# Kernel tuning notes

Hardware: AMD Instinct MI355X
Metric: run time of the kernel (lower is better)

The kernel has to match this reference:

```python
import jax, jax.numpy as jnp
import numpy as np

FIR = (1.0, 3.0, 3.0, 1.0)

def _fir_kernel():
    k = jnp.array(FIR, dtype=jnp.float32)
    k = jnp.outer(k, k)
    return k / jnp.sum(k)  # gain = 1

def setup_inputs() -> dict:
    key = jax.random.key(0)
    k1, k2, k3 = jax.random.split(key, 3)
    N, C, H, W = 8, 512, 64, 64
    return {
        "hidden_states": jax.random.normal(k1, (N, C, H, W), jnp.float32),
        "weight": jax.random.normal(k2, (512, 512, 3, 3), jnp.float32) * 0.02,
        "bias": jax.random.normal(k3, (512,), jnp.float32) * 0.01,
    }

def reference(hidden_states, weight, bias):
    # FirDownsample2D forward, use_conv=True, factor=2, fir_kernel=(1,3,3,1).
    # pad_value = kH - factor + (convW - 1) = 4 - 2 + 2 = 4 -> pad = (2, 2)
    k = _fir_kernel()  # [4,4], normalized
    C = hidden_states.shape[1]
    # upfirdn2d_native with up=1, down=1: pad spatially then per-channel
    # cross-correlation with the FLIPPED kernel (== true convolution).
    kf = jnp.flip(k, (0, 1)).astype(hidden_states.dtype)
    kf = jnp.broadcast_to(kf[None, None], (C, 1, 4, 4))  # depthwise [C,1,4,4]
    y = jax.lax.conv_general_dilated(
        hidden_states, kf, window_strides=(1, 1), padding=[(2, 2), (2, 2)],
        dimension_numbers=("NCHW", "OIHW", "NCHW"), feature_group_count=C)
    # y: [N, C, H+1, W+1]; fused 3x3 conv, stride=factor=2, no padding.
    out = jax.lax.conv_general_dilated(
        y, weight, window_strides=(2, 2), padding="VALID",
        dimension_numbers=("NCHW", "OIHW", "NCHW"))  # [N, Cout, H//2, W//2]
    return out + bias[None, :, None, None]
```

## Files before the change

### kernel.cpp

```cpp
#include <hip/hip_runtime.h>
#include <stdint.h>

#define CI 512
#define CO 512
#define HI 64
#define WI 64
#define HY 65
#define NB 8

typedef __bf16 bf16x8 __attribute__((ext_vector_type(8)));
typedef float f32x4 __attribute__((ext_vector_type(4)));

__device__ __forceinline__ unsigned short f2bf(float f) {
  unsigned int u = __float_as_uint(f);
  return (unsigned short)((u + 0x7fffu + ((u >> 16) & 1u)) >> 16);
}

__device__ __forceinline__ void async16(void* lds, const void* g) {
  __builtin_amdgcn_global_load_lds(
      (const __attribute__((address_space(1))) uint32_t*)g,
      (__attribute__((address_space(3))) uint32_t*)lds, 16, 0, 0);
}

#define CT 32
#define RT 13

__global__ __launch_bounds__(256) void fir_kernel(const float* __restrict__ x,
                                                  unsigned short* __restrict__ yt) {
  __shared__ float raw[CT][WI + 1];
  __shared__ float hrow[4][HY][CT];

  const int tid = threadIdx.x;
  const int bid = blockIdx.x;
  const int n = bid / 80;
  const int rem = bid % 80;
  const int c0 = (rem / 5) * CT;
  const int r0 = (rem % 5) * RT;

  const float* xb = x + ((size_t)n * CI + c0) * (HI * WI);

  const int lc = tid >> 3;
  const int lq = tid & 7;
  const int c = tid & (CT - 1);
  const int sb = tid >> 5;

  auto stage = [&](int hr) {
    __syncthreads();
    if ((unsigned)hr < (unsigned)HI) {
      const float* rowp = xb + ((size_t)lc * HI + hr) * WI;
      float4 a = *(const float4*)&rowp[lq * 4];
      float4 b = *(const float4*)&rowp[(lq + 8) * 4];
      raw[lc][lq * 4 + 0] = a.x; raw[lc][lq * 4 + 1] = a.y;
      raw[lc][lq * 4 + 2] = a.z; raw[lc][lq * 4 + 3] = a.w;
      raw[lc][(lq + 8) * 4 + 0] = b.x; raw[lc][(lq + 8) * 4 + 1] = b.y;
      raw[lc][(lq + 8) * 4 + 2] = b.z; raw[lc][(lq + 8) * 4 + 3] = b.w;
    }
    __syncthreads();
    const int slot = hr & 3;
    if ((unsigned)hr < (unsigned)HI) {
#pragma unroll
      for (int k = 0; k < 9; k++) {
        const int s = sb + (k << 3);
        if (s < HY) {
          float v = 0.f;
          if (s >= 2) v += raw[c][s - 2];
          if (s >= 1) v += 3.f * raw[c][s - 1];
          if (s <= 63) v += 3.f * raw[c][s];
          if (s <= 62) v += raw[c][s + 1];
          hrow[slot][s][c] = v;
        }
      }
    } else {
#pragma unroll
      for (int k = 0; k < 9; k++) {
        const int s = sb + (k << 3);
        if (s < HY) hrow[slot][s][c] = 0.f;
      }
    }
  };

  stage(r0 - 2);
  stage(r0 - 1);
  stage(r0);

  for (int i = 0; i < RT; i++) {
    const int r = r0 + i;
    stage(r + 1);
    __syncthreads();
    const int q0 = (r - 2) & 3, q1 = (r - 1) & 3, q2 = r & 3, q3 = (r + 1) & 3;
    unsigned short* yo = yt + (((size_t)n * HY + r) * HY) * CI + c0 + c;
#pragma unroll
    for (int k = 0; k < 9; k++) {
      const int s = sb + (k << 3);
      if (s < HY) {
        const float y = (hrow[q0][s][c] + 3.f * hrow[q1][s][c] +
                         3.f * hrow[q2][s][c] + hrow[q3][s][c]) * (1.f / 64.f);
        yo[(size_t)s * CI] = f2bf(y);
      }
    }
  }
}

__global__ __launch_bounds__(256) void wt_kernel(const float* __restrict__ w,
                                                 unsigned short* __restrict__ wtb) {
  const int gid = blockIdx.x * 256 + threadIdx.x;
  const int ci = gid & (CI - 1);
  const int co = gid >> 9;
  const float* src = w + ((size_t)co * CI + ci) * 9;
#pragma unroll
  for (int t = 0; t < 9; t++) {
    wtb[((size_t)t * CO + co) * CI + ci] = f2bf(src[t]);
  }
}

__global__ __launch_bounds__(256) void init_kernel(const float* __restrict__ bias,
                                                   float* __restrict__ out) {
  const int gid = blockIdx.x * 256 + threadIdx.x;
  const float bv = bias[(gid >> 8) & 511];
  float4 v = {bv, bv, bv, bv};
  *(float4*)(out + (size_t)gid * 4) = v;
}

__global__ __launch_bounds__(512, 2) void conv_kernel(
    const unsigned short* __restrict__ wtb,
    const unsigned short* __restrict__ yt,
    float* __restrict__ out) {
  __shared__ unsigned short Alds[3][128 * 64];
  __shared__ unsigned short Blds[3][256 * 64];

  const int tid = threadIdx.x;
  const int xcd = blockIdx.x & 7;
  const int j = blockIdx.x >> 3;
  const int pos_tile = xcd * 4 + (j >> 3);
  const int variant = j & 7;
  const int co_t = (variant >> 1) << 7;
  const int split = variant & 1;
  const int ks0 = split * 36;
  const int m0 = pos_tile << 8;
  const int n = m0 >> 10;

  uint32_t aoff[2];
#pragma unroll
  for (int i = 0; i < 2; i++) {
    const int ch = tid + i * 512;
    const int row = ch >> 3, s = ch & 7;
    aoff[i] = (uint32_t)((co_t + row) * CI + ((s ^ (row & 7)) << 3));
  }
  uint32_t boff[4];
#pragma unroll
  for (int i = 0; i < 4; i++) {
    const int ch = tid + i * 512;
    const int p = ch >> 3, s = ch & 7;
    const int pos = m0 + p;
    const int ho = (pos & 1023) >> 5, wo = pos & 31;
    boff[i] = (uint32_t)(((n * HY + 2 * ho) * HY + 2 * wo) * CI + ((s ^ (p & 7)) << 3));
  }

  auto stg = [&](unsigned short* Ab, unsigned short* Bb, int gks) {
    const int tap = gks >> 3;
    const int ci0 = (gks & 7) << 6;
    const int kh = tap / 3, kw = tap - kh * 3;
    const unsigned short* wsrc = wtb + (size_t)tap * (CO * CI) + ci0;
    const unsigned short* ysrc = yt + (size_t)(kh * HY + kw) * CI + ci0;
#pragma unroll
    for (int i = 0; i < 2; i++)
      async16(Ab + (size_t)(tid + i * 512) * 8, wsrc + aoff[i]);
#pragma unroll
    for (int i = 0; i < 4; i++)
      async16(Bb + (size_t)(tid + i * 512) * 8, ysrc + boff[i]);
  };

  const int wv = tid >> 6;
  const int wcoW = (wv >> 2) << 6;
  const int wposW = (wv & 3) << 6;
  const int l = tid & 63;
  const int ll = l & 15, kg = l >> 4;
  const int a7 = ll & 7;

  int aidx[4][2], bidx[4][2];
#pragma unroll
  for (int m = 0; m < 4; m++)
#pragma unroll
    for (int kk = 0; kk < 2; kk++)
      aidx[m][kk] = (wcoW + m * 16 + ll) * 64 + ((((kk << 2) | kg) ^ a7) << 3);
#pragma unroll
  for (int nf = 0; nf < 4; nf++)
#pragma unroll
    for (int kk = 0; kk < 2; kk++)
      bidx[nf][kk] = (wposW + nf * 16 + ll) * 64 + ((((kk << 2) | kg) ^ a7) << 3);

  f32x4 acc[4][4] = {};

  stg(&Alds[0][0], &Blds[0][0], ks0);
  stg(&Alds[1][0], &Blds[1][0], ks0 + 1);
  asm volatile("s_waitcnt vmcnt(6)" ::: "memory");
  __builtin_amdgcn_s_barrier();

#define COMPUTE(CUR)                                                        \
  {                                                                         \
    const unsigned short* Ac = &Alds[CUR][0];                               \
    const unsigned short* Bc = &Blds[CUR][0];                               \
    _Pragma("unroll") for (int kk = 0; kk < 2; kk++) {                      \
      const bf16x8 a0 = *(const bf16x8*)(Ac + aidx[0][kk]);                 \
      const bf16x8 a1 = *(const bf16x8*)(Ac + aidx[1][kk]);                 \
      const bf16x8 a2 = *(const bf16x8*)(Ac + aidx[2][kk]);                 \
      const bf16x8 a3 = *(const bf16x8*)(Ac + aidx[3][kk]);                 \
      const bf16x8 b0 = *(const bf16x8*)(Bc + bidx[0][kk]);                 \
      const bf16x8 b1 = *(const bf16x8*)(Bc + bidx[1][kk]);                 \
      const bf16x8 b2 = *(const bf16x8*)(Bc + bidx[2][kk]);                 \
      const bf16x8 b3 = *(const bf16x8*)(Bc + bidx[3][kk]);                 \
      __builtin_amdgcn_s_setprio(1);                                        \
      _Pragma("unroll") for (int m = 0; m < 4; m++) {                       \
        const bf16x8 am = (m == 0) ? a0 : (m == 1) ? a1 : (m == 2) ? a2 : a3; \
        acc[m][0] = __builtin_amdgcn_mfma_f32_16x16x32_bf16(am, b0, acc[m][0], 0, 0, 0); \
        acc[m][1] = __builtin_amdgcn_mfma_f32_16x16x32_bf16(am, b1, acc[m][1], 0, 0, 0); \
        acc[m][2] = __builtin_amdgcn_mfma_f32_16x16x32_bf16(am, b2, acc[m][2], 0, 0, 0); \
        acc[m][3] = __builtin_amdgcn_mfma_f32_16x16x32_bf16(am, b3, acc[m][3], 0, 0, 0); \
      }                                                                     \
      __builtin_amdgcn_s_setprio(0);                                        \
    }                                                                       \
  }

#define ITER(CUR, NXT, KSL)                                                 \
  {                                                                         \
    const int ksl = (KSL);                                                  \
    if (ksl + 2 < 36) stg(&Alds[NXT][0], &Blds[NXT][0], ks0 + ksl + 2);     \
    COMPUTE(CUR);                                                           \
    if (ksl < 34) {                                                         \
      asm volatile("s_waitcnt vmcnt(6)" ::: "memory");                      \
      __builtin_amdgcn_s_barrier();                                         \
    } else if (ksl == 34) {                                                 \
      asm volatile("s_waitcnt vmcnt(0)" ::: "memory");                      \
      __builtin_amdgcn_s_barrier();                                         \
    }                                                                       \
  }

  for (int kb = 0; kb < 36; kb += 3) {
    ITER(0, 2, kb);
    ITER(1, 0, kb + 1);
    ITER(2, 1, kb + 2);
  }
#undef ITER
#undef COMPUTE

#pragma unroll
  for (int m = 0; m < 4; m++) {
#pragma unroll
    for (int r = 0; r < 4; r++) {
      const int co = co_t + wcoW + m * 16 + kg * 4 + r;
      float* orow = out + ((size_t)n * CO + co) * 1024;
#pragma unroll
      for (int nf = 0; nf < 4; nf++) {
        const int pos = m0 + wposW + nf * 16 + ll;
        atomicAdd(orow + (pos & 1023), acc[m][nf][r]);
      }
    }
  }
}

extern "C" void kernel_launch(void* const* d_in, const int* in_sizes, int n_in,
                              void* d_out, int out_size, void* d_ws, size_t ws_size,
                              hipStream_t stream) {
  const float* x = (const float*)d_in[0];
  const float* w = (const float*)d_in[1];
  const float* bias = (const float*)d_in[2];
  float* out = (float*)d_out;

  unsigned short* yt = (unsigned short*)d_ws;
  unsigned short* wtb = yt + (size_t)NB * HY * HY * CI;

  fir_kernel<<<NB * (CI / CT) * 5, 256, 0, stream>>>(x, yt);
  wt_kernel<<<(CO * CI) / 256, 256, 0, stream>>>(w, wtb);
  init_kernel<<<4096, 256, 0, stream>>>(bias, out);
  conv_kernel<<<256, 512, 0, stream>>>(wtb, yt, out);
}
```

Baseline: 103.5 us.

## Enlarge conv tile to 256x256 with 4-way split-K and ping-pong double buffering

The conv kernel's block tile grows from 128 output channels x 256 positions to 256 x 256, so each block reuses its staged weight and activation tiles across more MFMAs. Split-K goes from 2-way to 4-way to keep the same block count. The triple-buffered LDS pipeline becomes a double buffer with a barrier-separated schedule that interleaves LDS fragment loads with MFMA bursts under raised priority, and the XCD-aware block mapping is dropped. In exchange it doubles the per-wave accumulator registers, adds twice as many atomic output adds, and prefetches only one k-step ahead with many more barriers per step.

```diff
diff --git a/kernel.cpp b/kernel.cpp
--- a/kernel.cpp
+++ b/kernel.cpp
@@ -21,6 +21,9 @@
       (const __attribute__((address_space(1))) uint32_t*)g,
       (__attribute__((address_space(3))) uint32_t*)lds, 16, 0, 0);
 }
+
+#define FENCE asm volatile("" ::: "memory")
+#define BAR do { FENCE; __builtin_amdgcn_s_barrier(); FENCE; } while (0)
 
 #define CT 32
 #define RT 13
@@ -125,134 +128,142 @@
     const unsigned short* __restrict__ wtb,
     const unsigned short* __restrict__ yt,
     float* __restrict__ out) {
-  __shared__ unsigned short Alds[3][128 * 64];
-  __shared__ unsigned short Blds[3][256 * 64];
+  __shared__ unsigned short Ylds[2][256 * 64];
+  __shared__ unsigned short Wlds[2][256 * 64];
 
   const int tid = threadIdx.x;
-  const int xcd = blockIdx.x & 7;
-  const int j = blockIdx.x >> 3;
-  const int pos_tile = xcd * 4 + (j >> 3);
-  const int variant = j & 7;
-  const int co_t = (variant >> 1) << 7;
-  const int split = variant & 1;
-  const int ks0 = split * 36;
+  const int pos_tile = blockIdx.x >> 3;
+  const int variant = blockIdx.x & 7;
+  const int co_t = (variant & 1) << 8;
+  const int split = variant >> 1;
+  const int ks0 = split * 18;
   const int m0 = pos_tile << 8;
   const int n = m0 >> 10;
 
-  uint32_t aoff[2];
-#pragma unroll
-  for (int i = 0; i < 2; i++) {
-    const int ch = tid + i * 512;
-    const int row = ch >> 3, s = ch & 7;
-    aoff[i] = (uint32_t)((co_t + row) * CI + ((s ^ (row & 7)) << 3));
-  }
-  uint32_t boff[4];
+  uint32_t yoff[4], woff[4];
 #pragma unroll
   for (int i = 0; i < 4; i++) {
     const int ch = tid + i * 512;
     const int p = ch >> 3, s = ch & 7;
     const int pos = m0 + p;
     const int ho = (pos & 1023) >> 5, wo = pos & 31;
-    boff[i] = (uint32_t)(((n * HY + 2 * ho) * HY + 2 * wo) * CI + ((s ^ (p & 7)) << 3));
-  }
-
-  auto stg = [&](unsigned short* Ab, unsigned short* Bb, int gks) {
+    yoff[i] = (uint32_t)(((n * HY + 2 * ho) * HY + 2 * wo) * CI + ((s ^ (p & 7)) << 3));
+    woff[i] = (uint32_t)((co_t + p) * CI + ((s ^ (p & 7)) << 3));
+  }
+
+  auto stg = [&](unsigned short* Yb, unsigned short* Wb, int gks) {
     const int tap = gks >> 3;
     const int ci0 = (gks & 7) << 6;
     const int kh = tap / 3, kw = tap - kh * 3;
-    const unsigned short* wsrc = wtb + (size_t)tap * (CO * CI) + ci0;
-    const unsigned short* ysrc = yt + (size_t)(kh * HY + kw) * CI + ci0;
-#pragma unroll
-    for (int i = 0; i < 2; i++)
-      async16(Ab + (size_t)(tid + i * 512) * 8, wsrc + aoff[i]);
+    const unsigned short* ys = yt + (size_t)(kh * HY + kw) * CI + ci0;
+    const unsigned short* ws = wtb + (size_t)tap * (CO * CI) + ci0;
 #pragma unroll
     for (int i = 0; i < 4; i++)
-      async16(Bb + (size_t)(tid + i * 512) * 8, ysrc + boff[i]);
+      async16(Yb + (size_t)(tid + i * 512) * 8, ys + yoff[i]);
+#pragma unroll
+    for (int i = 0; i < 4; i++)
+      async16(Wb + (size_t)(tid + i * 512) * 8, ws + woff[i]);
   };
 
   const int wv = tid >> 6;
-  const int wcoW = (wv >> 2) << 6;
-  const int wposW = (wv & 3) << 6;
+  const int mg = wv >> 2;
+  const int ng = wv & 3;
   const int l = tid & 63;
   const int ll = l & 15, kg = l >> 4;
-  const int a7 = ll & 7;
-
-  int aidx[4][2], bidx[4][2];
-#pragma unroll
-  for (int m = 0; m < 4; m++)
+  const int sw = ll & 7;
+
+  int yidx[8][2], widx[4][2];
+#pragma unroll
+  for (int mi = 0; mi < 8; mi++)
 #pragma unroll
     for (int kk = 0; kk < 2; kk++)
-      aidx[m][kk] = (wcoW + m * 16 + ll) * 64 + ((((kk << 2) | kg) ^ a7) << 3);
+      yidx[mi][kk] = (mg * 128 + mi * 16 + ll) * 64 + ((((kk << 2) | kg) ^ sw) << 3);
 #pragma unroll
   for (int nf = 0; nf < 4; nf++)
 #pragma unroll
     for (int kk = 0; kk < 2; kk++)
-      bidx[nf][kk] = (wposW + nf * 16 + ll) * 64 + ((((kk << 2) | kg) ^ a7) << 3);
-
-  f32x4 acc[4][4] = {};
-
-  stg(&Alds[0][0], &Blds[0][0], ks0);
-  stg(&Alds[1][0], &Blds[1][0], ks0 + 1);
-  asm volatile("s_waitcnt vmcnt(6)" ::: "memory");
-  __builtin_amdgcn_s_barrier();
-
-#define COMPUTE(CUR)                                                        \
-  {                                                                         \
-    const unsigned short* Ac = &Alds[CUR][0];                               \
-    const unsigned short* Bc = &Blds[CUR][0];                               \
-    _Pragma("unroll") for (int kk = 0; kk < 2; kk++) {                      \
-      const bf16x8 a0 = *(const bf16x8*)(Ac + aidx[0][kk]);                 \
-      const bf16x8 a1 = *(const bf16x8*)(Ac + aidx[1][kk]);                 \
-      const bf16x8 a2 = *(const bf16x8*)(Ac + aidx[2][kk]);                 \
-      const bf16x8 a3 = *(const bf16x8*)(Ac + aidx[3][kk]);                 \
-      const bf16x8 b0 = *(const bf16x8*)(Bc + bidx[0][kk]);                 \
-      const bf16x8 b1 = *(const bf16x8*)(Bc + bidx[1][kk]);                 \
-      const bf16x8 b2 = *(const bf16x8*)(Bc + bidx[2][kk]);                 \
-      const bf16x8 b3 = *(const bf16x8*)(Bc + bidx[3][kk]);                 \
-      __builtin_amdgcn_s_setprio(1);                                        \
-      _Pragma("unroll") for (int m = 0; m < 4; m++) {                       \
-        const bf16x8 am = (m == 0) ? a0 : (m == 1) ? a1 : (m == 2) ? a2 : a3; \
-        acc[m][0] = __builtin_amdgcn_mfma_f32_16x16x32_bf16(am, b0, acc[m][0], 0, 0, 0); \
-        acc[m][1] = __builtin_amdgcn_mfma_f32_16x16x32_bf16(am, b1, acc[m][1], 0, 0, 0); \
-        acc[m][2] = __builtin_amdgcn_mfma_f32_16x16x32_bf16(am, b2, acc[m][2], 0, 0, 0); \
-        acc[m][3] = __builtin_amdgcn_mfma_f32_16x16x32_bf16(am, b3, acc[m][3], 0, 0, 0); \
-      }                                                                     \
-      __builtin_amdgcn_s_setprio(0);                                        \
-    }                                                                       \
-  }
-
-#define ITER(CUR, NXT, KSL)                                                 \
-  {                                                                         \
-    const int ksl = (KSL);                                                  \
-    if (ksl + 2 < 36) stg(&Alds[NXT][0], &Blds[NXT][0], ks0 + ksl + 2);     \
-    COMPUTE(CUR);                                                           \
-    if (ksl < 34) {                                                         \
-      asm volatile("s_waitcnt vmcnt(6)" ::: "memory");                      \
-      __builtin_amdgcn_s_barrier();                                         \
-    } else if (ksl == 34) {                                                 \
-      asm volatile("s_waitcnt vmcnt(0)" ::: "memory");                      \
-      __builtin_amdgcn_s_barrier();                                         \
-    }                                                                       \
-  }
-
-  for (int kb = 0; kb < 36; kb += 3) {
-    ITER(0, 2, kb);
-    ITER(1, 0, kb + 1);
-    ITER(2, 1, kb + 2);
-  }
-#undef ITER
-#undef COMPUTE
-
-#pragma unroll
-  for (int m = 0; m < 4; m++) {
-#pragma unroll
-    for (int r = 0; r < 4; r++) {
-      const int co = co_t + wcoW + m * 16 + kg * 4 + r;
-      float* orow = out + ((size_t)n * CO + co) * 1024;
-#pragma unroll
-      for (int nf = 0; nf < 4; nf++) {
-        const int pos = m0 + wposW + nf * 16 + ll;
-        atomicAdd(orow + (pos & 1023), acc[m][nf][r]);
+      widx[nf][kk] = (ng * 64 + nf * 16 + ll) * 64 + ((((kk << 2) | kg) ^ sw) << 3);
+
+  f32x4 acc[8][4] = {};
+
+#define LDF(base, idx) (*(const bf16x8*)((base) + (idx)))
+#define MF4(MI, YV, WA, WB, WC, WD)                                              \
+  acc[MI][0] = __builtin_amdgcn_mfma_f32_16x16x32_bf16(WA, YV, acc[MI][0], 0, 0, 0); \
+  acc[MI][1] = __builtin_amdgcn_mfma_f32_16x16x32_bf16(WB, YV, acc[MI][1], 0, 0, 0); \
+  acc[MI][2] = __builtin_amdgcn_mfma_f32_16x16x32_bf16(WC, YV, acc[MI][2], 0, 0, 0); \
+  acc[MI][3] = __builtin_amdgcn_mfma_f32_16x16x32_bf16(WD, YV, acc[MI][3], 0, 0, 0);
+
+#define KSTEP(CUR, DO_STAGE, GKS)                                         \
+  {                                                                       \
+    const unsigned short* Yc = &Ylds[CUR][0];                             \
+    const unsigned short* Wc = &Wlds[CUR][0];                             \
+            \
+    bf16x8 w0 = LDF(Wc, widx[0][0]), w1 = LDF(Wc, widx[1][0]);            \
+    bf16x8 w2 = LDF(Wc, widx[2][0]), w3 = LDF(Wc, widx[3][0]);            \
+    bf16x8 y0 = LDF(Yc, yidx[0][0]), y1 = LDF(Yc, yidx[1][0]);            \
+    bf16x8 y2 = LDF(Yc, yidx[2][0]), y3 = LDF(Yc, yidx[3][0]);            \
+    bf16x8 v0, v1, v2, v3;                                                \
+    if (DO_STAGE) stg(&Ylds[(CUR) ^ 1][0], &Wlds[(CUR) ^ 1][0], (GKS));   \
+    BAR;                                                                  \
+    __builtin_amdgcn_s_setprio(1);                                        \
+    MF4(0, y0, w0, w1, w2, w3); MF4(1, y1, w0, w1, w2, w3);               \
+    MF4(2, y2, w0, w1, w2, w3); MF4(3, y3, w0, w1, w2, w3);               \
+    __builtin_amdgcn_s_setprio(0);                                        \
+    BAR;                                                                  \
+                                        \
+    y0 = LDF(Yc, yidx[4][0]); y1 = LDF(Yc, yidx[5][0]);                   \
+    y2 = LDF(Yc, yidx[6][0]); y3 = LDF(Yc, yidx[7][0]);                   \
+    v0 = LDF(Wc, widx[0][1]); v1 = LDF(Wc, widx[1][1]);                   \
+    v2 = LDF(Wc, widx[2][1]); v3 = LDF(Wc, widx[3][1]);                   \
+    BAR;                                                                  \
+    __builtin_amdgcn_s_setprio(1);                                        \
+    MF4(4, y0, w0, w1, w2, w3); MF4(5, y1, w0, w1, w2, w3);               \
+    MF4(6, y2, w0, w1, w2, w3); MF4(7, y3, w0, w1, w2, w3);               \
+    __builtin_amdgcn_s_setprio(0);                                        \
+    BAR;                                                                  \
+                                                \
+    y0 = LDF(Yc, yidx[0][1]); y1 = LDF(Yc, yidx[1][1]);                   \
+    y2 = LDF(Yc, yidx[2][1]); y3 = LDF(Yc, yidx[3][1]);                   \
+    BAR;                                                                  \
+    __builtin_amdgcn_s_setprio(1);                                        \
+    MF4(0, y0, v0, v1, v2, v3); MF4(1, y1, v0, v1, v2, v3);               \
+    MF4(2, y2, v0, v1, v2, v3); MF4(3, y3, v0, v1, v2, v3);               \
+    __builtin_amdgcn_s_setprio(0);                                        \
+    BAR;                                                                  \
+                      \
+    y0 = LDF(Yc, yidx[4][1]); y1 = LDF(Yc, yidx[5][1]);                   \
+    y2 = LDF(Yc, yidx[6][1]); y3 = LDF(Yc, yidx[7][1]);                   \
+    if (DO_STAGE) { asm volatile("s_waitcnt vmcnt(0)" ::: "memory"); }    \
+    BAR;                                                                  \
+    __builtin_amdgcn_s_setprio(1);                                        \
+    MF4(4, y0, v0, v1, v2, v3); MF4(5, y1, v0, v1, v2, v3);               \
+    MF4(6, y2, v0, v1, v2, v3); MF4(7, y3, v0, v1, v2, v3);               \
+    __builtin_amdgcn_s_setprio(0);                                        \
+    BAR;                                                                  \
+  }
+
+  stg(&Ylds[0][0], &Wlds[0][0], ks0);
+  asm volatile("s_waitcnt vmcnt(0)" ::: "memory");
+  BAR;
+
+#pragma unroll 1
+  for (int u = 0; u < 9; u++) {
+    KSTEP(0, true, ks0 + 2 * u + 1);
+    KSTEP(1, (u < 8), ks0 + 2 * u + 2);
+  }
+#undef KSTEP
+#undef MF4
+#undef LDF
+
+#pragma unroll
+  for (int mi = 0; mi < 8; mi++) {
+#pragma unroll
+    for (int nf = 0; nf < 4; nf++) {
+#pragma unroll
+      for (int r = 0; r < 4; r++) {
+        const int co = co_t + ng * 64 + nf * 16 + kg * 4 + r;
+        const int pos = m0 + mg * 128 + mi * 16 + ll;
+        atomicAdd(out + ((size_t)n * CO + co) * 1024 + (pos & 1023), acc[mi][nf][r]);
       }
     }
   }
```

New measurement: 130.1 us. 25.7% more time.
